# Performance work log

Hardware: AMD Instinct MI355X
Metric: run time of the kernel (lower is better)

## Reference

```python
import jax, jax.numpy as jnp
import numpy as np
import math

HIDDEN = 4096
N_HEADS = 32
HEAD_DIM = HIDDEN // N_HEADS
MAX_POS = 4096
BASE = 10000.0
NEG_INF = jnp.finfo(jnp.float32).min


def rotate_half(x):
    x1, x2 = jnp.split(x, 2, axis=-1)
    return jnp.concatenate((-x2, x1), axis=-1)


def rope_tables(seq_len, dtype=jnp.float32):
    inv_freq = 1.0 / (BASE ** (jnp.arange(0, HEAD_DIM, 2, dtype=jnp.float32) / HEAD_DIM))
    t = jnp.arange(seq_len, dtype=jnp.float32)
    freqs = jnp.einsum('i,j->ij', t, inv_freq)  # [S, D/2]
    emb = jnp.concatenate((freqs, freqs), axis=-1)  # [S, D]
    return jnp.cos(emb).astype(dtype), jnp.sin(emb).astype(dtype)


def setup_inputs() -> dict:
    key = jax.random.key(0)
    k1, k2, k3 = jax.random.split(key, 3)
    bsz, q_len = 2, 2048
    hidden_states = jax.random.normal(k1, (bsz, q_len, HIDDEN), dtype=jnp.float32)
    # causal additive mask [bsz, 1, q, q]: 0 on/below diag, large-negative above
    causal = jnp.triu(jnp.full((q_len, q_len), NEG_INF, dtype=jnp.float32), k=1)
    attention_mask = jnp.broadcast_to(causal[None, None], (bsz, 1, q_len, q_len))
    position_ids = jnp.broadcast_to(jnp.arange(q_len, dtype=jnp.int64)[None], (bsz, q_len))
    W_pack = jax.random.normal(k2, (3 * HIDDEN, HIDDEN), dtype=jnp.float32) * (1.0 / math.sqrt(HIDDEN))
    W_o = jax.random.normal(k3, (HIDDEN, HIDDEN), dtype=jnp.float32) * (1.0 / math.sqrt(HIDDEN))
    return {"hidden_states": hidden_states, "attention_mask": attention_mask,
            "position_ids": position_ids, "W_pack": W_pack, "W_o": W_o}


def reference(hidden_states, attention_mask, position_ids, W_pack, W_o):
    bsz, q_len, _ = hidden_states.shape
    proj = jnp.einsum('bsh,oh->bso', hidden_states, W_pack)  # [B,S,3H]
    q, k, v = jnp.split(proj, 3, axis=-1)
    def shape(x):
        return x.reshape(bsz, q_len, N_HEADS, HEAD_DIM).transpose(0, 2, 1, 3)  # [B,nH,S,D]
    q, k, v = shape(q), shape(k), shape(v)
    cos, sin = rope_tables(q_len, hidden_states.dtype)
    cos = cos[position_ids][:, None]  # [B,1,S,D]
    sin = sin[position_ids][:, None]
    q = q * cos + rotate_half(q) * sin
    k = k * cos + rotate_half(k) * sin
    scores = jnp.einsum('bhqd,bhkd->bhqk', q, k) / math.sqrt(HEAD_DIM)
    scores = scores + attention_mask
    scores = jnp.maximum(scores, NEG_INF)
    w = jax.nn.softmax(scores.astype(jnp.float32), axis=-1).astype(q.dtype)
    out = jnp.einsum('bhqk,bhkd->bhqd', w, v)
    out = out.transpose(0, 2, 1, 3).reshape(bsz, q_len, HIDDEN)
    return jnp.einsum('bsh,oh->bso', out, W_o)
```

## Files before the change

### kernel.cpp

```cpp
#include <hip/hip_runtime.h>
#include <hip/hip_bf16.h>

typedef __bf16 bf16x8 __attribute__((ext_vector_type(8)));
typedef float f32x4 __attribute__((ext_vector_type(4)));

#define HIDDEN 4096
#define NH 32
#define HD 128
#define SEQ 2048
#define BATCH 2
#define MTOT 4096
#define QKV 12288

__device__ __forceinline__ void async16(const void* g, void* l) {
    __builtin_amdgcn_global_load_lds(
        (const __attribute__((address_space(1))) void*)(uintptr_t)g,
        (__attribute__((address_space(3))) void*)(uint32_t)(uintptr_t)l,
        16, 0, 0);
}

__device__ __forceinline__ uint4 ld8(const __hip_bfloat16* p) { return *(const uint4*)p; }
__device__ __forceinline__ uint4 ld8(const float* p) {
    float4 a = *(const float4*)p;
    float4 b = *(const float4*)(p + 4);
    __hip_bfloat16 t[8];
    t[0] = __float2bfloat16(a.x); t[1] = __float2bfloat16(a.y);
    t[2] = __float2bfloat16(a.z); t[3] = __float2bfloat16(a.w);
    t[4] = __float2bfloat16(b.x); t[5] = __float2bfloat16(b.y);
    t[6] = __float2bfloat16(b.z); t[7] = __float2bfloat16(b.w);
    return *(uint4*)t;
}

__device__ __forceinline__ void stc(__hip_bfloat16* C, size_t i, float v) { C[i] = __float2bfloat16(v); }
__device__ __forceinline__ void stc(float* C, size_t i, float v) { C[i] = v; }

__global__ __launch_bounds__(256) void cvt_bf16(const float* __restrict__ src,
                                                __hip_bfloat16* __restrict__ dst, int n8) {
    int i = blockIdx.x * 256 + threadIdx.x;
    if (i < n8) *(uint4*)&dst[(size_t)i * 8] = ld8(&src[(size_t)i * 8]);
}

template <typename TC>
__global__ __launch_bounds__(512) void gemm_256(const __hip_bfloat16* __restrict__ A,
                                                const __hip_bfloat16* __restrict__ Bt,
                                                TC* __restrict__ C,
                                                int M, int N, int K, int lda) {
    __shared__ __align__(16) __hip_bfloat16 As[4][256][32];
    __shared__ __align__(16) __hip_bfloat16 Bs[4][256][32];
    const int bn = blockIdx.x * 256, bm = blockIdx.y * 256;
    const int tid = threadIdx.x, wave = tid >> 6, lane = tid & 63;
    const int wm = wave >> 2, wn = wave & 3;
    const int row16 = lane & 15, quad = lane >> 4;
    const int lr = lane >> 2;
    const int lc = (lane & 3) * 8;
    const __hip_bfloat16* Ab = A + (size_t)(bm + wave * 16 + lr) * lda + lc;
    const __hip_bfloat16* Bb = Bt + (size_t)(bn + wave * 16 + lr) * K + lc;
    const int NT = K >> 5;

    f32x4 acc[8][4] = {};

    auto stage = [&](int t) {
        const int s = t & 3;
        const int kt = t << 5;
        async16(Ab + kt,                     &As[s][wave * 16][0]);
        async16(Ab + (size_t)128 * lda + kt, &As[s][wave * 16 + 128][0]);
        async16(Bb + kt,                     &Bs[s][wave * 16][0]);
        async16(Bb + (size_t)128 * K + kt,   &Bs[s][wave * 16 + 128][0]);
    };

    stage(0); stage(1); stage(2);

    for (int t = 0; t < NT; ++t) {
        const int s = t & 3;
        const int rem = NT - 1 - t;
        if (rem >= 2)      asm volatile("s_waitcnt vmcnt(8)" ::: "memory");
        else if (rem == 1) asm volatile("s_waitcnt vmcnt(4)" ::: "memory");
        else               asm volatile("s_waitcnt vmcnt(0)" ::: "memory");
        __builtin_amdgcn_s_barrier();
        __builtin_amdgcn_sched_barrier(0);
        if (t + 3 < NT) stage(t + 3);
        bf16x8 af[8], bf[4];
#pragma unroll
        for (int i = 0; i < 8; ++i)
            af[i] = *(const bf16x8*)&As[s][wm * 128 + i * 16 + row16][quad * 8];
#pragma unroll
        for (int j = 0; j < 4; ++j)
            bf[j] = *(const bf16x8*)&Bs[s][wn * 64 + j * 16 + row16][quad * 8];
        __builtin_amdgcn_s_setprio(1);
#pragma unroll
        for (int i = 0; i < 8; ++i)
#pragma unroll
            for (int j = 0; j < 4; ++j)
                acc[i][j] = __builtin_amdgcn_mfma_f32_16x16x32_bf16(af[i], bf[j], acc[i][j], 0, 0, 0);
        __builtin_amdgcn_s_setprio(0);
    }

    const int col0 = bn + wn * 64 + row16;
    const int row0 = bm + wm * 128 + quad * 4;
#pragma unroll
    for (int i = 0; i < 8; ++i)
#pragma unroll
        for (int j = 0; j < 4; ++j)
#pragma unroll
            for (int rg = 0; rg < 4; ++rg)
                stc(C, (size_t)(row0 + i * 16 + rg) * N + col0 + j * 16, acc[i][j][rg]);
}

template <typename TA, typename TB, typename TC>
__global__ __launch_bounds__(256) void gemm_bt(const TA* __restrict__ A,
                                               const TB* __restrict__ Bt,
                                               TC* __restrict__ C,
                                               int M, int N, int K, int lda) {
    __shared__ __align__(16) __hip_bfloat16 As[128][32];
    __shared__ __align__(16) __hip_bfloat16 Bs[128][32];
    const int bn = blockIdx.x * 128, bm = blockIdx.y * 128;
    const int tid = threadIdx.x, wave = tid >> 6, lane = tid & 63;
    const int wm = (wave >> 1) * 64, wn = (wave & 1) * 64;
    const int row16 = lane & 15, quad = lane >> 4;
    const int arow = tid >> 2;
    const int acol = (tid & 3) * 8;

    f32x4 acc[4][4] = {};

    for (int kt = 0; kt < K; kt += 32) {
        __syncthreads();
#pragma unroll
        for (int it = 0; it < 2; ++it) {
            int r = arow + it * 64;
            *(uint4*)&As[r][acol] = ld8(&A[(size_t)(bm + r) * lda + kt + acol]);
            *(uint4*)&Bs[r][acol] = ld8(&Bt[(size_t)(bn + r) * K + kt + acol]);
        }
        __syncthreads();
        bf16x8 af[4], bf[4];
#pragma unroll
        for (int i = 0; i < 4; ++i) af[i] = *(const bf16x8*)&As[wm + i * 16 + row16][quad * 8];
#pragma unroll
        for (int j = 0; j < 4; ++j) bf[j] = *(const bf16x8*)&Bs[wn + j * 16 + row16][quad * 8];
#pragma unroll
        for (int i = 0; i < 4; ++i)
#pragma unroll
            for (int j = 0; j < 4; ++j)
                acc[i][j] = __builtin_amdgcn_mfma_f32_16x16x32_bf16(af[i], bf[j], acc[i][j], 0, 0, 0);
    }
    const int col0 = bn + wn + row16;
    const int row0 = bm + wm + quad * 4;
#pragma unroll
    for (int i = 0; i < 4; ++i)
#pragma unroll
        for (int j = 0; j < 4; ++j)
#pragma unroll
            for (int rg = 0; rg < 4; ++rg)
                stc(C, (size_t)(row0 + i * 16 + rg) * N + col0 + j * 16, acc[i][j][rg]);
}

__global__ __launch_bounds__(256) void rope_kernel(__hip_bfloat16* __restrict__ proj) {
    int t = blockIdx.x * 256 + threadIdx.x;
    int j = t & 63;
    int head = (t >> 6) & 31;
    int mat = (t >> 11) & 1;
    int row = t >> 12;
    int pos = row & (SEQ - 1);
    float invf = __expf(-(float)j * 0.14391156514261f);
    float ang = (float)pos * invf;
    float rev = ang * 0.15915494309189535f;
    rev -= floorf(rev);
    float arad = rev * 6.283185307179586f;
    float sn = __sinf(arad);
    float cs = __cosf(arad);
    if (mat == 0) {
        sn *= 0.08838834764831845f;
        cs *= 0.08838834764831845f;
    }
    size_t base = (size_t)row * QKV + mat * HIDDEN + head * HD + j;
    float x1 = __bfloat162float(proj[base]);
    float x2 = __bfloat162float(proj[base + 64]);
    proj[base]      = __float2bfloat16(x1 * cs - x2 * sn);
    proj[base + 64] = __float2bfloat16(x2 * cs + x1 * sn);
}

__global__ __launch_bounds__(256) void transpose_v(const __hip_bfloat16* __restrict__ proj,
                                                   __hip_bfloat16* __restrict__ vtg) {
    __shared__ __hip_bfloat16 Ls[64][132];
    const int st = blockIdx.x, bh = blockIdx.y;
    const int b = bh >> 5, h = bh & 31;
    const int s0 = st << 6;
    const int tid = threadIdx.x;
    const __hip_bfloat16* vb = proj + (size_t)b * SEQ * QKV + 2 * HIDDEN + h * HD;
    for (int i = tid; i < 1024; i += 256) {
        int r = i >> 4, c = (i & 15) << 3;
        uint4 raw = *(const uint4*)&vb[(size_t)(s0 + r) * QKV + c];
        *(uint2*)&Ls[r][c]     = make_uint2(raw.x, raw.y);
        *(uint2*)&Ls[r][c + 4] = make_uint2(raw.z, raw.w);
    }
    __syncthreads();
    __hip_bfloat16* ob = vtg + (size_t)bh * HD * SEQ + s0;
    for (int t = tid; t < 1024; t += 256) {
        int d = t >> 3, sc = (t & 7) << 3;
        __hip_bfloat16 tmp[8];
#pragma unroll
        for (int x = 0; x < 8; ++x) tmp[x] = Ls[sc + x][d];
        *(uint4*)&ob[(size_t)d * SEQ + sc] = *(uint4*)tmp;
    }
}

__global__ __launch_bounds__(512) void attn_mfma(__hip_bfloat16* __restrict__ proj,
                                                 const __hip_bfloat16* __restrict__ vtg) {
    __shared__ __align__(16) __hip_bfloat16 Kf[2][16][512];
    __shared__ __align__(16) __hip_bfloat16 Vf[2][16][512];
    __shared__ __align__(16) __hip_bfloat16 Ps[8][32][72];
    const int nwg = gridDim.x * gridDim.y;
    const int f  = blockIdx.y * gridDim.x + blockIdx.x;
    const int f2 = (f & 7) * (nwg >> 3) + (f >> 3);
    const int qt = f2 & 7;
    const int bh = f2 >> 3;
    const int b = bh >> 5, h = bh & 31;
    const int q0 = qt << 8;
    const int tid = threadIdx.x, wave = tid >> 6, lane = tid & 63;
    const int row16 = lane & 15, quad = lane >> 4;

    __hip_bfloat16* qb = proj + (size_t)b * SEQ * QKV + h * HD;
    const __hip_bfloat16* kb = qb + HIDDEN;
    const __hip_bfloat16* vp = vtg + (size_t)bh * HD * SEQ;

    const int wbase = q0 + wave * 32;

    const int b0 = 2 * wave, b1 = 2 * wave + 1;
    const __hip_bfloat16* ks0 = kb + (size_t)((b0 >> 2) * 16 + row16) * QKV + (b0 & 3) * 32 + quad * 8;
    const __hip_bfloat16* ks1 = kb + (size_t)((b1 >> 2) * 16 + row16) * QKV + (b1 & 3) * 32 + quad * 8;
    const __hip_bfloat16* vs0 = vp + (size_t)((b0 >> 1) * 16 + row16) * SEQ + (b0 & 1) * 32 + quad * 8;
    const __hip_bfloat16* vs1 = vp + (size_t)((b1 >> 1) * 16 + row16) * SEQ + (b1 & 1) * 32 + quad * 8;

    auto stage = [&](int kt) {
        const int s = kt & 1;
        const int k0 = kt << 6;
        async16(ks0 + (size_t)k0 * QKV, &Kf[s][b0][0]);
        async16(ks1 + (size_t)k0 * QKV, &Kf[s][b1][0]);
        async16(vs0 + k0,               &Vf[s][b0][0]);
        async16(vs1 + k0,               &Vf[s][b1][0]);
    };

    bf16x8 qf[2][4];
#pragma unroll
    for (int qr = 0; qr < 2; ++qr) {
        const __hip_bfloat16* qrow = qb + (size_t)(wbase + qr * 16 + row16) * QKV + quad * 8;
#pragma unroll
        for (int s = 0; s < 4; ++s) qf[qr][s] = *(const bf16x8*)(qrow + s * 32);
    }

    f32x4 oa[2][8] = {};
    float m_i[2][4], l_i[2][4];
#pragma unroll
    for (int qr = 0; qr < 2; ++qr)
#pragma unroll
        for (int r = 0; r < 4; ++r) { m_i[qr][r] = -3.0e38f; l_i[qr][r] = 0.f; }

    stage(0);
    asm volatile("s_waitcnt vmcnt(0)" ::: "memory");
    __builtin_amdgcn_s_barrier();
    __builtin_amdgcn_sched_barrier(0);

    const int ktmax = 4 * qt + 3;
    for (int kt = 0; kt <= ktmax; ++kt) {
        const int s = kt & 1;
        const int k0 = kt << 6;
        if (kt < ktmax) stage(kt + 1);
        if (k0 <= wbase + 31) {
            f32x4 sf[2][4] = {};
#pragma unroll
            for (int nt = 0; nt < 4; ++nt) {
                bf16x8 kf[4];
#pragma unroll
                for (int ks = 0; ks < 4; ++ks)
                    kf[ks] = *(const bf16x8*)&Kf[s][nt * 4 + ks][lane * 8];
#pragma unroll
                for (int qr = 0; qr < 2; ++qr)
#pragma unroll
                    for (int ks = 0; ks < 4; ++ks)
                        sf[qr][nt] = __builtin_amdgcn_mfma_f32_16x16x32_bf16(qf[qr][ks], kf[ks], sf[qr][nt], 0, 0, 0);
            }
            if (k0 + 63 > wbase) {
#pragma unroll
                for (int qr = 0; qr < 2; ++qr)
#pragma unroll
                    for (int nt = 0; nt < 4; ++nt) {
                        int key = k0 + nt * 16 + row16;
#pragma unroll
                        for (int rg = 0; rg < 4; ++rg)
                            if (key > wbase + qr * 16 + quad * 4 + rg) sf[qr][nt][rg] = -3.0e38f;
                    }
            }
#pragma unroll
            for (int qr = 0; qr < 2; ++qr) {
                float alpha[4], rs[4];
#pragma unroll
                for (int rg = 0; rg < 4; ++rg) {
                    float mx = fmaxf(fmaxf(sf[qr][0][rg], sf[qr][1][rg]), fmaxf(sf[qr][2][rg], sf[qr][3][rg]));
#pragma unroll
                    for (int off = 8; off > 0; off >>= 1) mx = fmaxf(mx, __shfl_xor(mx, off));
                    float mn = fmaxf(m_i[qr][rg], mx);
                    alpha[rg] = __expf(m_i[qr][rg] - mn);
                    m_i[qr][rg] = mn;
                    rs[rg] = 0.f;
                }
#pragma unroll
                for (int nt = 0; nt < 4; ++nt)
#pragma unroll
                    for (int rg = 0; rg < 4; ++rg) {
                        float p = __expf(sf[qr][nt][rg] - m_i[qr][rg]);
                        rs[rg] += p;
                        Ps[wave][qr * 16 + quad * 4 + rg][nt * 16 + row16] = __float2bfloat16(p);
                    }
#pragma unroll
                for (int rg = 0; rg < 4; ++rg) {
#pragma unroll
                    for (int off = 8; off > 0; off >>= 1) rs[rg] += __shfl_xor(rs[rg], off);
                    l_i[qr][rg] = l_i[qr][rg] * alpha[rg] + rs[rg];
                }
#pragma unroll
                for (int dt = 0; dt < 8; ++dt)
#pragma unroll
                    for (int rg = 0; rg < 4; ++rg) oa[qr][dt][rg] *= alpha[rg];
            }
            __builtin_amdgcn_wave_barrier();
            bf16x8 pf[2][2];
#pragma unroll
            for (int qr = 0; qr < 2; ++qr) {
                pf[qr][0] = *(const bf16x8*)&Ps[wave][qr * 16 + row16][quad * 8];
                pf[qr][1] = *(const bf16x8*)&Ps[wave][qr * 16 + row16][32 + quad * 8];
            }
#pragma unroll
            for (int dt = 0; dt < 8; ++dt) {
                bf16x8 v0 = *(const bf16x8*)&Vf[s][dt * 2][lane * 8];
                bf16x8 v1 = *(const bf16x8*)&Vf[s][dt * 2 + 1][lane * 8];
#pragma unroll
                for (int qr = 0; qr < 2; ++qr) {
                    oa[qr][dt] = __builtin_amdgcn_mfma_f32_16x16x32_bf16(pf[qr][0], v0, oa[qr][dt], 0, 0, 0);
                    oa[qr][dt] = __builtin_amdgcn_mfma_f32_16x16x32_bf16(pf[qr][1], v1, oa[qr][dt], 0, 0, 0);
                }
            }
        }
        asm volatile("s_waitcnt vmcnt(0)" ::: "memory");
        __builtin_amdgcn_s_barrier();
        __builtin_amdgcn_sched_barrier(0);
    }
#pragma unroll
    for (int qr = 0; qr < 2; ++qr)
#pragma unroll
        for (int rg = 0; rg < 4; ++rg) {
            float inv = 1.0f / l_i[qr][rg];
            __hip_bfloat16* orow = qb + (size_t)(wbase + qr * 16 + quad * 4 + rg) * QKV;
#pragma unroll
            for (int dt = 0; dt < 8; ++dt)
                orow[dt * 16 + row16] = __float2bfloat16(oa[qr][dt][rg] * inv);
        }
}

extern "C" void kernel_launch(void* const* d_in, const int* in_sizes, int n_in,
                              void* d_out, int out_size, void* d_ws, size_t ws_size,
                              hipStream_t stream) {
    const float* hs = (const float*)d_in[0];
    const float* Wp = (const float*)d_in[3];
    const float* Wo = (const float*)d_in[4];
    float* out = (float*)d_out;

    const size_t SZ_PROJ = (size_t)MTOT * QKV;
    const size_t SZ_H    = (size_t)MTOT * HIDDEN;
    const size_t SZ_WP   = (size_t)QKV * HIDDEN;
    const size_t need = (SZ_PROJ + SZ_H + SZ_WP + SZ_H) * sizeof(__hip_bfloat16);

    __hip_bfloat16* proj = (__hip_bfloat16*)d_ws;

    if (ws_size >= need) {
        __hip_bfloat16* hsb = proj + SZ_PROJ;
        __hip_bfloat16* Wpb = hsb + SZ_H;
        __hip_bfloat16* Wob = Wpb + SZ_WP;
        __hip_bfloat16* vtg = hsb;

        cvt_bf16<<<dim3(SZ_H / 8 / 256), dim3(256), 0, stream>>>(hs, hsb, SZ_H / 8);
        cvt_bf16<<<dim3(SZ_WP / 8 / 256), dim3(256), 0, stream>>>(Wp, Wpb, SZ_WP / 8);
        cvt_bf16<<<dim3(SZ_H / 8 / 256), dim3(256), 0, stream>>>(Wo, Wob, SZ_H / 8);
        gemm_256<<<dim3(QKV / 256, MTOT / 256), dim3(512), 0, stream>>>(hsb, Wpb, proj, MTOT, QKV, HIDDEN, HIDDEN);
        rope_kernel<<<dim3((MTOT * 2 * NH * 64) / 256), dim3(256), 0, stream>>>(proj);
        transpose_v<<<dim3(SEQ / 64, BATCH * NH), dim3(256), 0, stream>>>(proj, vtg);
        attn_mfma<<<dim3(SEQ / 256, BATCH * NH), dim3(512), 0, stream>>>(proj, vtg);
        gemm_256<<<dim3(HIDDEN / 256, MTOT / 256), dim3(512), 0, stream>>>(proj, Wob, out, MTOT, HIDDEN, HIDDEN, QKV);
    } else {
        __hip_bfloat16* vtg = proj + SZ_PROJ;
        gemm_bt<<<dim3(QKV / 128, MTOT / 128), dim3(256), 0, stream>>>(hs, Wp, proj, MTOT, QKV, HIDDEN, HIDDEN);
        rope_kernel<<<dim3((MTOT * 2 * NH * 64) / 256), dim3(256), 0, stream>>>(proj);
        transpose_v<<<dim3(SEQ / 64, BATCH * NH), dim3(256), 0, stream>>>(proj, vtg);
        attn_mfma<<<dim3(SEQ / 256, BATCH * NH), dim3(512), 0, stream>>>(proj, vtg);
        gemm_bt<<<dim3(HIDDEN / 128, MTOT / 128), dim3(256), 0, stream>>>(proj, Wo, out, MTOT, HIDDEN, HIDDEN, QKV);
    }
}
```

Baseline: 1.199 ms.

## Use BK=64 double-buffered LDS tiles with XOR swizzle in bf16 GEMM

Changes the 256x256 GEMM from a 4-stage BK=32 pipeline to a 2-stage BK=64 pipeline. LDS rows become 64 elements wide, with a lane-XOR chunk swizzle on both the async global-to-LDS loads and the fragment reads, to avoid bank conflicts. This halves the number of barriers per K and makes each barrier cover more MFMAs. In exchange, prefetch depth drops to a single stage with a full vmcnt(0) wait each iteration, which may expose memory latency.

```diff
diff --git a/kernel.cpp b/kernel.cpp
--- a/kernel.cpp
+++ b/kernel.cpp
@@ -45,54 +45,58 @@
                                                 const __hip_bfloat16* __restrict__ Bt,
                                                 TC* __restrict__ C,
                                                 int M, int N, int K, int lda) {
-    __shared__ __align__(16) __hip_bfloat16 As[4][256][32];
-    __shared__ __align__(16) __hip_bfloat16 Bs[4][256][32];
+    __shared__ __align__(16) __hip_bfloat16 As[2][256][64];
+    __shared__ __align__(16) __hip_bfloat16 Bs[2][256][64];
     const int bn = blockIdx.x * 256, bm = blockIdx.y * 256;
     const int tid = threadIdx.x, wave = tid >> 6, lane = tid & 63;
     const int wm = wave >> 2, wn = wave & 3;
     const int row16 = lane & 15, quad = lane >> 4;
-    const int lr = lane >> 2;
-    const int lc = (lane & 3) * 8;
-    const __hip_bfloat16* Ab = A + (size_t)(bm + wave * 16 + lr) * lda + lc;
-    const __hip_bfloat16* Bb = Bt + (size_t)(bn + wave * 16 + lr) * K + lc;
-    const int NT = K >> 5;
+    const int srow = lane >> 3;
+    const int schunk = (lane & 7) ^ srow;
+    const __hip_bfloat16* Ab = A + (size_t)(bm + wave * 8 + srow) * lda + schunk * 8;
+    const __hip_bfloat16* Bb = Bt + (size_t)(bn + wave * 8 + srow) * K + schunk * 8;
+    const int NT = K >> 6;
 
     f32x4 acc[8][4] = {};
 
     auto stage = [&](int t) {
-        const int s = t & 3;
-        const int kt = t << 5;
-        async16(Ab + kt,                     &As[s][wave * 16][0]);
-        async16(Ab + (size_t)128 * lda + kt, &As[s][wave * 16 + 128][0]);
-        async16(Bb + kt,                     &Bs[s][wave * 16][0]);
-        async16(Bb + (size_t)128 * K + kt,   &Bs[s][wave * 16 + 128][0]);
+        const int s = t & 1;
+        const size_t kt = (size_t)t << 6;
+#pragma unroll
+        for (int k = 0; k < 4; ++k) {
+            async16(Ab + (size_t)(k * 64) * lda + kt, &As[s][k * 64 + wave * 8][0]);
+            async16(Bb + (size_t)(k * 64) * K  + kt, &Bs[s][k * 64 + wave * 8][0]);
+        }
     };
 
-    stage(0); stage(1); stage(2);
+    stage(0);
 
     for (int t = 0; t < NT; ++t) {
-        const int s = t & 3;
-        const int rem = NT - 1 - t;
-        if (rem >= 2)      asm volatile("s_waitcnt vmcnt(8)" ::: "memory");
-        else if (rem == 1) asm volatile("s_waitcnt vmcnt(4)" ::: "memory");
-        else               asm volatile("s_waitcnt vmcnt(0)" ::: "memory");
+        const int s = t & 1;
+        asm volatile("s_waitcnt vmcnt(0)" ::: "memory");
         __builtin_amdgcn_s_barrier();
+        if (t + 1 < NT) stage(t + 1);
         __builtin_amdgcn_sched_barrier(0);
-        if (t + 3 < NT) stage(t + 3);
-        bf16x8 af[8], bf[4];
-#pragma unroll
-        for (int i = 0; i < 8; ++i)
-            af[i] = *(const bf16x8*)&As[s][wm * 128 + i * 16 + row16][quad * 8];
-#pragma unroll
-        for (int j = 0; j < 4; ++j)
-            bf[j] = *(const bf16x8*)&Bs[s][wn * 64 + j * 16 + row16][quad * 8];
-        __builtin_amdgcn_s_setprio(1);
-#pragma unroll
-        for (int i = 0; i < 8; ++i)
+        const int pcb = (quad ^ (row16 & 7)) * 8;
+        const int pcb1 = ((4 + quad) ^ (row16 & 7)) * 8;
+#pragma unroll
+        for (int ks = 0; ks < 2; ++ks) {
+            const int pc = ks ? pcb1 : pcb;
+            bf16x8 af[8], bf[4];
+#pragma unroll
+            for (int i = 0; i < 8; ++i)
+                af[i] = *(const bf16x8*)&As[s][wm * 128 + i * 16 + row16][pc];
 #pragma unroll
             for (int j = 0; j < 4; ++j)
-                acc[i][j] = __builtin_amdgcn_mfma_f32_16x16x32_bf16(af[i], bf[j], acc[i][j], 0, 0, 0);
-        __builtin_amdgcn_s_setprio(0);
+                bf[j] = *(const bf16x8*)&Bs[s][wn * 64 + j * 16 + row16][pc];
+            __builtin_amdgcn_s_setprio(1);
+#pragma unroll
+            for (int i = 0; i < 8; ++i)
+#pragma unroll
+                for (int j = 0; j < 4; ++j)
+                    acc[i][j] = __builtin_amdgcn_mfma_f32_16x16x32_bf16(af[i], bf[j], acc[i][j], 0, 0, 0);
+            __builtin_amdgcn_s_setprio(0);
+        }
     }
 
     const int col0 = bn + wn * 64 + row16;
```

Result: faster. 1.110 ms (-7.4%).
